# Kernel tuning notes

Hardware: AMD Instinct MI355X
Metric: run time of the kernel (lower is better)

Reference implementation:

```python
import jax, jax.numpy as jnp
import numpy as np

EPS = 1e-7          # K.epsilon()
STRIDE = 1
ROUTINGS = 3


def squash(v, axis=-1):
    # Faithful to original: squash default axis=-1, which for preactivate
    # [B, oc, na, H, W] is the spatial W axis (as the source code computes).
    s2 = jnp.sum(v * v, axis=axis, keepdims=True)
    scale = s2 / (1.0 + s2) / jnp.sqrt(s2 + EPS)
    return scale * v


def setup_inputs() -> dict:
    key = jax.random.key(0)
    k1, k2 = jax.random.split(key, 2)
    B, H, Wd, ic, ia = 32, 32, 32, 8, 16
    k, oc, na = 3, 16, 16
    x = jax.random.normal(k1, (B, H, Wd, ic, ia), jnp.float32)
    # he_normal: std = sqrt(2 / fan_in), fan_in = kd*kh*kw*ci = ia*k*k*1
    std = np.sqrt(2.0 / (ia * k * k)).astype(np.float32)
    W = jax.random.normal(k2, (ia, k, k, 1, oc * na), jnp.float32) * std
    b = jnp.full((oc, na, 1, 1), 0.1, jnp.float32)
    return {"x": x, "W": W, "b": b}


def reference(x, W, b):
    B, H, Wd, ic, ia = x.shape
    oc, na = b.shape[0], b.shape[1]
    # Faithful raw reshape of input_tensor (NOT of input_transposed), as in source.
    xr = x.reshape(B, 1, ic * ia, H, Wd)
    # conv3d channels_first, kernel (kd,kh,kw,ci,co), strides (ia, s, s), valid.
    conv = jax.lax.conv_general_dilated(
        xr, W,
        window_strides=(ia, STRIDE, STRIDE),
        padding='VALID',
        dimension_numbers=('NCDHW', 'DHWIO', 'NCDHW'))
    # conv: [B, oc*na, ic, Hc, Wc]
    _, _, d, Hc, Wc = conv.shape  # d == ic
    votes = jnp.transpose(conv, (0, 2, 1, 3, 4)).reshape(B, ic, oc, na, Hc, Wc)
    biases = jnp.broadcast_to(b, (oc, na, Hc, Wc))
    logits = jnp.zeros((B, ic, oc, Hc, Wc), x.dtype)
    activation = None
    for i in range(ROUTINGS):  # fixed small trip count
        route = jax.nn.softmax(logits, axis=2)           # over output capsules
        # route [B,ic,oc,1,H,W] * votes [B,ic,oc,na,H,W], sum over ic
        preact = jnp.sum(route[:, :, :, None] * votes, axis=1) + biases
        activation = squash(preact, axis=-1)             # [B, oc, na, Hc, Wc]
        if i < ROUTINGS - 1:
            # agreement: sum over atoms axis (axis=3 of votes)
            logits = logits + jnp.sum(votes * activation[:, None], axis=3)
    # final transpose [0,3,4,1,2] -> [B, Hc, Wc, oc, na]
    return jnp.transpose(activation, (0, 3, 4, 1, 2))
```

## Files before the change

### kernel.cpp

```cpp
#include <hip/hip_runtime.h>
#include <hip/hip_bf16.h>

typedef float    f32x4  __attribute__((ext_vector_type(4)));
typedef float    f32x16 __attribute__((ext_vector_type(16)));
typedef _Float16 f16x8  __attribute__((ext_vector_type(8)));
typedef _Float16 f16x4  __attribute__((ext_vector_type(4)));
typedef _Float16 f16x2  __attribute__((ext_vector_type(2)));

#define VP 258
#define XP 132
#define AP 258

__global__ __launch_bounds__(256) void prep_wt_kernel(
    const float* __restrict__ W, _Float16* __restrict__ wt)
{
    const int k = blockIdx.x;
    const int t = threadIdx.x;
    wt[t * 144 + (k % 9) * 16 + (k / 9)] = (_Float16)W[k * 256 + t];
}

__global__ __launch_bounds__(1024, 4) void fused_kernel(
    const float* __restrict__ x, const _Float16* __restrict__ wt,
    const float* __restrict__ bias, float* __restrict__ out)
{
    const int bid = blockIdx.x;
    const int wid = (bid & 7) * 120 + (bid >> 3);
    const int b = wid / 30, h = wid - 30 * b;
    const int t = threadIdx.x;

    __shared__ _Float16 vlds[8 * 30 * VP];
    __shared__ union {
        _Float16 xs[3][36][XP];
        struct {
            _Float16 route16[8 * 16 * 32];
            _Float16 act16[30 * AP];
            float    s2buf[4][256];
        } rt;
    } u;

    {
        const float* xb = x + (size_t)b * 131072;
        f32x4 v0[2], v1[2];
        int p0s[2], rs[2], c4s[2];
        #pragma unroll
        for (int j = 0; j < 2; ++j) {
            int q = t + j * 1024;
            bool ok = q < 1536;
            int qq = ok ? q : 0;
            int g  = qq / 24;
            p0s[j] = g * 2;
            int rem = qq - g * 24;
            rs[j] = rem >> 3; c4s[j] = rem & 7;
            if (ok) {
                v0[j] = *(const f32x4*)(xb + p0s[j] * 1024 + (h + rs[j]) * 32 + c4s[j] * 4);
                v1[j] = *(const f32x4*)(xb + (p0s[j] + 1) * 1024 + (h + rs[j]) * 32 + c4s[j] * 4);
            }
        }
        if (t < 768) {
            int r = t / 256, rem = t - r * 256;
            int c = rem >> 6, pz = (rem & 63) * 2;
            *(f16x2*)&u.xs[r][32 + c][pz] = f16x2{(_Float16)0.f, (_Float16)0.f};
        }
        #pragma unroll
        for (int j = 0; j < 2; ++j) {
            if (t + j * 1024 < 1536) {
                #pragma unroll
                for (int c = 0; c < 4; ++c)
                    *(f16x2*)&u.xs[rs[j]][c4s[j] * 4 + c][p0s[j]] =
                        f16x2{(_Float16)v0[j][c], (_Float16)v1[j][c]};
            }
        }
    }
    __syncthreads();

    const int lane = t & 63, wv = t >> 6;
    const int l31  = lane & 31;
    const int kb   = lane >> 5;
    const int ct   = wv >> 1, dh = wv & 1;
    const int oaC  = ct * 32 + l31;

    {
        f16x8 bf[9];
        const _Float16* wp = wt + (size_t)oaC * 144 + kb * 8;
        #pragma unroll
        for (int s = 0; s < 9; ++s) bf[s] = *(const f16x8*)(wp + s * 16);

        #pragma unroll
        for (int dd = 0; dd < 4; ++dd) {
            f32x16 acc = {};
            #pragma unroll
            for (int s = 0; s < 9; ++s) {
                const int kh = s / 3, kw = s - 3 * (s / 3);
                const _Float16* ap = &u.xs[kh][l31 + kw][dh * 64 + dd * 16 + kb * 8];
                f16x4 lo = *(const f16x4*)(ap);
                f16x4 hi = *(const f16x4*)(ap + 4);
                f16x8 af = __builtin_shufflevector(lo, hi, 0, 1, 2, 3, 4, 5, 6, 7);
                acc = __builtin_amdgcn_mfma_f32_32x32x16_f16(af, bf[s], acc, 0, 0, 0);
            }
            const int d = dh * 4 + dd;
            #pragma unroll
            for (int r = 0; r < 16; ++r) {
                const int wr = (r & 3) + 8 * (r >> 2) + 4 * kb;
                if (wr < 30) vlds[(d * 30 + wr) * VP + oaC] = (_Float16)acc[r];
            }
        }
    }
    __syncthreads();

    const int oa = t & 255, wq = t >> 8;
    const int o  = oa >> 4;
    const int wbase = wq * 8;
    const int nw = (wq == 3) ? 6 : 8;
    const float bias_t = bias[oa];
    const int iA = t / 30, wA = t - iA * 30;

    float lreg[16];
    #pragma unroll
    for (int oo = 0; oo < 16; ++oo) lreg[oo] = 0.f;

    float pre[8];
    float scale = 0.f;

    for (int it = 0; it < 3; ++it) {
        if (it > 0) {
            if (t < 240) {
                float m = lreg[0];
                #pragma unroll
                for (int oo = 1; oo < 16; ++oo) m = fmaxf(m, lreg[oo]);
                float e[16], ssum = 0.f;
                #pragma unroll
                for (int oo = 0; oo < 16; ++oo) { e[oo] = __expf(lreg[oo] - m); ssum += e[oo]; }
                float inv = 1.f / ssum;
                #pragma unroll
                for (int oo = 0; oo < 16; ++oo)
                    u.rt.route16[(iA * 16 + oo) * 32 + wA] = (_Float16)(e[oo] * inv);
            }
            __syncthreads();
        }

        #pragma unroll
        for (int w = 0; w < 8; ++w) pre[w] = bias_t;
        if (it == 0) {
            #pragma unroll
            for (int i = 0; i < 8; ++i) {
                const _Float16* vrow = &vlds[(i * 30 + wbase) * VP + oa];
                #pragma unroll
                for (int w = 0; w < 8; ++w)
                    if (w < nw) pre[w] = fmaf(0.0625f, (float)vrow[w * VP], pre[w]);
            }
        } else {
            #pragma unroll
            for (int i = 0; i < 8; ++i) {
                const _Float16* vrow = &vlds[(i * 30 + wbase) * VP + oa];
                const _Float16* rr   = &u.rt.route16[(i * 16 + o) * 32 + wbase];
                #pragma unroll
                for (int w = 0; w < 8; ++w)
                    if (w < nw) pre[w] = fmaf((float)rr[w], (float)vrow[w * VP], pre[w]);
            }
        }
        float s2p = 0.f;
        #pragma unroll
        for (int w = 0; w < 8; ++w)
            if (w < nw) s2p = fmaf(pre[w], pre[w], s2p);
        u.rt.s2buf[wq][oa] = s2p;
        __syncthreads();
        float s2 = u.rt.s2buf[0][oa] + u.rt.s2buf[1][oa]
                 + u.rt.s2buf[2][oa] + u.rt.s2buf[3][oa];
        scale = s2 / ((1.f + s2) * sqrtf(s2 + 1e-7f));

        if (it < 2) {
            #pragma unroll
            for (int w = 0; w < 8; ++w)
                if (w < nw) u.rt.act16[(wbase + w) * AP + oa] = (_Float16)(scale * pre[w]);
            __syncthreads();
            if (t < 240) {
                const _Float16* vrow = &vlds[(iA * 30 + wA) * VP];
                const _Float16* arow = &u.rt.act16[wA * AP];
                #pragma unroll
                for (int oo = 0; oo < 16; ++oo) {
                    float s = 0.f;
                    #pragma unroll
                    for (int k = 0; k < 8; ++k) {
                        f16x2 v2 = *(const f16x2*)&vrow[oo * 16 + 2 * k];
                        f16x2 a2 = *(const f16x2*)&arow[oo * 16 + 2 * k];
                        s = fmaf((float)v2[0], (float)a2[0], s);
                        s = fmaf((float)v2[1], (float)a2[1], s);
                    }
                    if (it == 0) lreg[oo] = s; else lreg[oo] += s;
                }
            }
        }
    }

    float* ob = out + (size_t)((b * 30 + h) * 30) * 256;
    #pragma unroll
    for (int w = 0; w < 8; ++w)
        if (w < nw) ob[(wbase + w) * 256 + oa] = scale * pre[w];
}

extern "C" void kernel_launch(void* const* d_in, const int* in_sizes, int n_in,
                              void* d_out, int out_size, void* d_ws, size_t ws_size,
                              hipStream_t stream)
{
    const float* x    = (const float*)d_in[0];
    const float* Wt   = (const float*)d_in[1];
    const float* bias = (const float*)d_in[2];
    float* out = (float*)d_out;
    _Float16* wt_h = (_Float16*)d_ws;

    prep_wt_kernel<<<dim3(144), 256, 0, stream>>>(Wt, wt_h);
    fused_kernel<<<dim3(960), 1024, 0, stream>>>(x, wt_h, bias, out);
}
```

Before: 75.87 us.

## Make fused capsule kernel persistent with prefetch of next row's input

```diff
diff --git a/kernel.cpp b/kernel.cpp
--- a/kernel.cpp
+++ b/kernel.cpp
@@ -4,11 +4,10 @@
 typedef float    f32x4  __attribute__((ext_vector_type(4)));
 typedef float    f32x16 __attribute__((ext_vector_type(16)));
 typedef _Float16 f16x8  __attribute__((ext_vector_type(8)));
-typedef _Float16 f16x4  __attribute__((ext_vector_type(4)));
 typedef _Float16 f16x2  __attribute__((ext_vector_type(2)));
 
 #define VP 258
-#define XP 132
+#define XP 136
 #define AP 258
 
 __global__ __launch_bounds__(256) void prep_wt_kernel(
@@ -19,14 +18,13 @@
     wt[t * 144 + (k % 9) * 16 + (k / 9)] = (_Float16)W[k * 256 + t];
 }
 
-__global__ __launch_bounds__(1024, 4) void fused_kernel(
+__global__ __launch_bounds__(1024) void fused_kernel(
     const float* __restrict__ x, const _Float16* __restrict__ wt,
     const float* __restrict__ bias, float* __restrict__ out)
 {
-    const int bid = blockIdx.x;
-    const int wid = (bid & 7) * 120 + (bid >> 3);
-    const int b = wid / 30, h = wid - 30 * b;
-    const int t = threadIdx.x;
+    const int kblk = blockIdx.x;
+    const int t    = threadIdx.x;
+    const int njobs = (kblk < 192) ? 4 : 3;
 
     __shared__ _Float16 vlds[8 * 30 * VP];
     __shared__ union {
@@ -38,52 +36,67 @@
         } rt;
     } u;
 
+    const int lane = t & 63, wv = t >> 6;
+    const int l31 = lane & 31, kb = lane >> 5;
+    const int ct = wv >> 1, dh = wv & 1;
+    const int oaC = ct * 32 + l31;
+
+    const int oa = t & 255, wq = t >> 8;
+    const int o = oa >> 4;
+    const int wbase = wq * 8;
+    const int nw = (wq == 3) ? 6 : 8;
+    const float bias_t = bias[oa];
+    const int iA = t / 30, wA = t - iA * 30;
+
+    const bool ok1 = (t < 512);
+    const int g0 = t / 24,          p00 = g0 * 2;
+    const int rem0 = t - g0 * 24,   r0 = rem0 >> 3, c40 = rem0 & 7;
+    const int q1 = t + 1024;
+    const int g1 = q1 / 24,         p01 = g1 * 2;
+    const int rem1 = q1 - g1 * 24,  r1 = rem1 >> 3, c41 = rem1 & 7;
+
+    f16x8 bf[9];
     {
+        const _Float16* wp = wt + (size_t)oaC * 144 + kb * 8;
+        #pragma unroll
+        for (int s = 0; s < 9; ++s) bf[s] = *(const f16x8*)(wp + s * 16);
+    }
+
+    f32x4 v00, v01, v10, v11;
+    {
+        const int j = kblk;
+        const int wid = (j & 7) * 120 + (j >> 3);
+        const int b = wid / 30, h = wid - 30 * b;
         const float* xb = x + (size_t)b * 131072;
-        f32x4 v0[2], v1[2];
-        int p0s[2], rs[2], c4s[2];
-        #pragma unroll
-        for (int j = 0; j < 2; ++j) {
-            int q = t + j * 1024;
-            bool ok = q < 1536;
-            int qq = ok ? q : 0;
-            int g  = qq / 24;
-            p0s[j] = g * 2;
-            int rem = qq - g * 24;
-            rs[j] = rem >> 3; c4s[j] = rem & 7;
-            if (ok) {
-                v0[j] = *(const f32x4*)(xb + p0s[j] * 1024 + (h + rs[j]) * 32 + c4s[j] * 4);
-                v1[j] = *(const f32x4*)(xb + (p0s[j] + 1) * 1024 + (h + rs[j]) * 32 + c4s[j] * 4);
-            }
-        }
+        v00 = *(const f32x4*)(xb + p00 * 1024 + (h + r0) * 32 + c40 * 4);
+        v01 = *(const f32x4*)(xb + (p00 + 1) * 1024 + (h + r0) * 32 + c40 * 4);
+        if (ok1) {
+            v10 = *(const f32x4*)(xb + p01 * 1024 + (h + r1) * 32 + c41 * 4);
+            v11 = *(const f32x4*)(xb + (p01 + 1) * 1024 + (h + r1) * 32 + c41 * 4);
+        }
+    }
+
+    for (int jj = 0; jj < njobs; ++jj) {
+        const int j = kblk + jj * 256;
+        const int wid = (j & 7) * 120 + (j >> 3);
+        const int b = wid / 30, h = wid - 30 * b;
+
+        if (jj > 0) __syncthreads();
+
         if (t < 768) {
             int r = t / 256, rem = t - r * 256;
             int c = rem >> 6, pz = (rem & 63) * 2;
             *(f16x2*)&u.xs[r][32 + c][pz] = f16x2{(_Float16)0.f, (_Float16)0.f};
         }
         #pragma unroll
-        for (int j = 0; j < 2; ++j) {
-            if (t + j * 1024 < 1536) {
-                #pragma unroll
-                for (int c = 0; c < 4; ++c)
-                    *(f16x2*)&u.xs[rs[j]][c4s[j] * 4 + c][p0s[j]] =
-                        f16x2{(_Float16)v0[j][c], (_Float16)v1[j][c]};
-            }
-        }
-    }
-    __syncthreads();
-
-    const int lane = t & 63, wv = t >> 6;
-    const int l31  = lane & 31;
-    const int kb   = lane >> 5;
-    const int ct   = wv >> 1, dh = wv & 1;
-    const int oaC  = ct * 32 + l31;
-
-    {
-        f16x8 bf[9];
-        const _Float16* wp = wt + (size_t)oaC * 144 + kb * 8;
-        #pragma unroll
-        for (int s = 0; s < 9; ++s) bf[s] = *(const f16x8*)(wp + s * 16);
+        for (int c = 0; c < 4; ++c)
+            *(f16x2*)&u.xs[r0][c40 * 4 + c][p00] = f16x2{(_Float16)v00[c], (_Float16)v01[c]};
+        if (ok1) {
+            #pragma unroll
+            for (int c = 0; c < 4; ++c)
+                *(f16x2*)&u.xs[r1][c41 * 4 + c][p01] = f16x2{(_Float16)v10[c], (_Float16)v11[c]};
+        }
+        __syncthreads();
 
         #pragma unroll
         for (int dd = 0; dd < 4; ++dd) {
@@ -91,10 +104,7 @@
             #pragma unroll
             for (int s = 0; s < 9; ++s) {
                 const int kh = s / 3, kw = s - 3 * (s / 3);
-                const _Float16* ap = &u.xs[kh][l31 + kw][dh * 64 + dd * 16 + kb * 8];
-                f16x4 lo = *(const f16x4*)(ap);
-                f16x4 hi = *(const f16x4*)(ap + 4);
-                f16x8 af = __builtin_shufflevector(lo, hi, 0, 1, 2, 3, 4, 5, 6, 7);
+                f16x8 af = *(const f16x8*)&u.xs[kh][l31 + kw][dh * 64 + dd * 16 + kb * 8];
                 acc = __builtin_amdgcn_mfma_f32_32x32x16_f16(af, bf[s], acc, 0, 0, 0);
             }
             const int d = dh * 4 + dd;
@@ -104,98 +114,105 @@
                 if (wr < 30) vlds[(d * 30 + wr) * VP + oaC] = (_Float16)acc[r];
             }
         }
-    }
-    __syncthreads();
-
-    const int oa = t & 255, wq = t >> 8;
-    const int o  = oa >> 4;
-    const int wbase = wq * 8;
-    const int nw = (wq == 3) ? 6 : 8;
-    const float bias_t = bias[oa];
-    const int iA = t / 30, wA = t - iA * 30;
-
-    float lreg[16];
-    #pragma unroll
-    for (int oo = 0; oo < 16; ++oo) lreg[oo] = 0.f;
-
-    float pre[8];
-    float scale = 0.f;
-
-    for (int it = 0; it < 3; ++it) {
-        if (it > 0) {
-            if (t < 240) {
-                float m = lreg[0];
+        __syncthreads();
+
+        if (jj + 1 < njobs) {
+            const int jn = kblk + (jj + 1) * 256;
+            const int widn = (jn & 7) * 120 + (jn >> 3);
+            const int bn = widn / 30, hn = widn - 30 * bn;
+            const float* xb = x + (size_t)bn * 131072;
+            v00 = *(const f32x4*)(xb + p00 * 1024 + (hn + r0) * 32 + c40 * 4);
+            v01 = *(const f32x4*)(xb + (p00 + 1) * 1024 + (hn + r0) * 32 + c40 * 4);
+            if (ok1) {
+                v10 = *(const f32x4*)(xb + p01 * 1024 + (hn + r1) * 32 + c41 * 4);
+                v11 = *(const f32x4*)(xb + (p01 + 1) * 1024 + (hn + r1) * 32 + c41 * 4);
+            }
+        }
+
+        float lreg[16];
+        float pre[8];
+        float scale = 0.f;
+
+        for (int it = 0; it < 3; ++it) {
+            if (it > 0) {
+                if (t < 240) {
+                    float m = lreg[0];
+                    #pragma unroll
+                    for (int oo = 1; oo < 16; ++oo) m = fmaxf(m, lreg[oo]);
+                    float e[16], ssum = 0.f;
+                    #pragma unroll
+                    for (int oo = 0; oo < 16; ++oo) { e[oo] = __expf(lreg[oo] - m); ssum += e[oo]; }
+                    float inv = 1.f / ssum;
+                    #pragma unroll
+                    for (int oo = 0; oo < 16; ++oo)
+                        u.rt.route16[(iA * 16 + oo) * 32 + wA] = (_Float16)(e[oo] * inv);
+                }
+                __syncthreads();
+            }
+
+            #pragma unroll
+            for (int w = 0; w < 8; ++w) pre[w] = bias_t;
+            if (it == 0) {
                 #pragma unroll
-                for (int oo = 1; oo < 16; ++oo) m = fmaxf(m, lreg[oo]);
-                float e[16], ssum = 0.f;
+                for (int i = 0; i < 8; ++i) {
+                    const _Float16* vrow = &vlds[(i * 30 + wbase) * VP + oa];
+                    #pragma unroll
+                    for (int w = 0; w < 8; ++w)
+                        if (w < nw) pre[w] = fmaf(0.0625f, (float)vrow[w * VP], pre[w]);
+                }
+            } else {
                 #pragma unroll
-                for (int oo = 0; oo < 16; ++oo) { e[oo] = __expf(lreg[oo] - m); ssum += e[oo]; }
-                float inv = 1.f / ssum;
-                #pragma unroll
-                for (int oo = 0; oo < 16; ++oo)
-                    u.rt.route16[(iA * 16 + oo) * 32 + wA] = (_Float16)(e[oo] * inv);
-            }
+                for (int i = 0; i < 8; ++i) {
+                    const _Float16* vrow = &vlds[(i * 30 + wbase) * VP + oa];
+                    const _Float16* rr   = &u.rt.route16[(i * 16 + o) * 32 + wbase];
+                    #pragma unroll
+                    for (int w = 0; w < 8; ++w)
+                        if (w < nw) pre[w] = fmaf((float)rr[w], (float)vrow[w * VP], pre[w]);
+                }
+            }
+            float s2p = 0.f;
+            #pragma unroll
+            for (int w = 0; w < 8; ++w)
+                if (w < nw) s2p = fmaf(pre[w], pre[w], s2p);
+            u.rt.s2buf[wq][oa] = s2p;
             __syncthreads();
-        }
-
-        #pragma unroll
-        for (int w = 0; w < 8; ++w) pre[w] = bias_t;
-        if (it == 0) {
-            #pragma unroll
-            for (int i = 0; i < 8; ++i) {
-                const _Float16* vrow = &vlds[(i * 30 + wbase) * VP + oa];
+            float s2 = u.rt.s2buf[0][oa] + u.rt.s2buf[1][oa]
+                     + u.rt.s2buf[2][oa] + u.rt.s2buf[3][oa];
+            scale = s2 / ((1.f + s2) * sqrtf(s2 + 1e-7f));
+
+            if (it < 2) {
                 #pragma unroll
                 for (int w = 0; w < 8; ++w)
-                    if (w < nw) pre[w] = fmaf(0.0625f, (float)vrow[w * VP], pre[w]);
-            }
-        } else {
-            #pragma unroll
-            for (int i = 0; i < 8; ++i) {
-                const _Float16* vrow = &vlds[(i * 30 + wbase) * VP + oa];
-                const _Float16* rr   = &u.rt.route16[(i * 16 + o) * 32 + wbase];
-                #pragma unroll
-                for (int w = 0; w < 8; ++w)
-                    if (w < nw) pre[w] = fmaf((float)rr[w], (float)vrow[w * VP], pre[w]);
-            }
-        }
-        float s2p = 0.f;
+                    if (w < nw) u.rt.act16[(wbase + w) * AP + oa] = (_Float16)(scale * pre[w]);
+                __syncthreads();
+                if (t < 240) {
+                    const _Float16* vrow = &vlds[(iA * 30 + wA) * VP];
+                    const _Float16* arow = &u.rt.act16[wA * AP];
+                    #pragma unroll
+                    for (int oo = 0; oo < 16; ++oo) {
+                        float s = 0.f;
+                        #pragma unroll
+                        for (int kk = 0; kk < 8; ++kk) {
+                            f16x2 v2 = *(const f16x2*)&vrow[oo * 16 + 2 * kk];
+                            f16x2 a2 = *(const f16x2*)&arow[oo * 16 + 2 * kk];
+#if __has_builtin(__builtin_amdgcn_fdot2)
+                            s = __builtin_amdgcn_fdot2(v2, a2, s, false);
+#else
+                            s = fmaf((float)v2[0], (float)a2[0], s);
+                            s = fmaf((float)v2[1], (float)a2[1], s);
+#endif
+                        }
+                        if (it == 0) lreg[oo] = s; else lreg[oo] += s;
+                    }
+                }
+            }
+        }
+
+        float* ob = out + (size_t)((b * 30 + h) * 30) * 256;
         #pragma unroll
         for (int w = 0; w < 8; ++w)
-            if (w < nw) s2p = fmaf(pre[w], pre[w], s2p);
-        u.rt.s2buf[wq][oa] = s2p;
-        __syncthreads();
-        float s2 = u.rt.s2buf[0][oa] + u.rt.s2buf[1][oa]
-                 + u.rt.s2buf[2][oa] + u.rt.s2buf[3][oa];
-        scale = s2 / ((1.f + s2) * sqrtf(s2 + 1e-7f));
-
-        if (it < 2) {
-            #pragma unroll
-            for (int w = 0; w < 8; ++w)
-                if (w < nw) u.rt.act16[(wbase + w) * AP + oa] = (_Float16)(scale * pre[w]);
-            __syncthreads();
-            if (t < 240) {
-                const _Float16* vrow = &vlds[(iA * 30 + wA) * VP];
-                const _Float16* arow = &u.rt.act16[wA * AP];
-                #pragma unroll
-                for (int oo = 0; oo < 16; ++oo) {
-                    float s = 0.f;
-                    #pragma unroll
-                    for (int k = 0; k < 8; ++k) {
-                        f16x2 v2 = *(const f16x2*)&vrow[oo * 16 + 2 * k];
-                        f16x2 a2 = *(const f16x2*)&arow[oo * 16 + 2 * k];
-                        s = fmaf((float)v2[0], (float)a2[0], s);
-                        s = fmaf((float)v2[1], (float)a2[1], s);
-                    }
-                    if (it == 0) lreg[oo] = s; else lreg[oo] += s;
-                }
-            }
-        }
+            if (w < nw) ob[(wbase + w) * 256 + oa] = scale * pre[w];
     }
-
-    float* ob = out + (size_t)((b * 30 + h) * 30) * 256;
-    #pragma unroll
-    for (int w = 0; w < 8; ++w)
-        if (w < nw) ob[(wbase + w) * 256 + oa] = scale * pre[w];
 }
 
 extern "C" void kernel_launch(void* const* d_in, const int* in_sizes, int n_in,
@@ -209,5 +226,5 @@
     _Float16* wt_h = (_Float16*)d_ws;
 
     prep_wt_kernel<<<dim3(144), 256, 0, stream>>>(Wt, wt_h);
-    fused_kernel<<<dim3(960), 1024, 0, stream>>>(x, wt_h, bias, out);
+    fused_kernel<<<dim3(256), 1024, 0, stream>>>(x, wt_h, bias, out);
 }
```

Result: slower. 179.2 us (+136.3%).

## Remap routing phase to two atoms per thread with vectorized LDS and fdot2

Applied to the files above, without the earlier changes.

```diff
diff --git a/kernel.cpp b/kernel.cpp
--- a/kernel.cpp
+++ b/kernel.cpp
@@ -1,15 +1,17 @@
 #include <hip/hip_runtime.h>
 #include <hip/hip_bf16.h>
 
+typedef float    f32x2  __attribute__((ext_vector_type(2)));
 typedef float    f32x4  __attribute__((ext_vector_type(4)));
 typedef float    f32x16 __attribute__((ext_vector_type(16)));
 typedef _Float16 f16x8  __attribute__((ext_vector_type(8)));
 typedef _Float16 f16x4  __attribute__((ext_vector_type(4)));
 typedef _Float16 f16x2  __attribute__((ext_vector_type(2)));
 
-#define VP 258
+#define VP 264
 #define XP 132
-#define AP 258
+#define AP 264
+#define RP 36
 
 __global__ __launch_bounds__(256) void prep_wt_kernel(
     const float* __restrict__ W, _Float16* __restrict__ wt)
@@ -28,13 +30,13 @@
     const int b = wid / 30, h = wid - 30 * b;
     const int t = threadIdx.x;
 
-    __shared__ _Float16 vlds[8 * 30 * VP];
-    __shared__ union {
+    __shared__ alignas(16) _Float16 vlds[8 * 30 * VP];
+    __shared__ alignas(16) union {
         _Float16 xs[3][36][XP];
         struct {
-            _Float16 route16[8 * 16 * 32];
+            _Float16 route16[8 * 16 * RP];
             _Float16 act16[30 * AP];
-            float    s2buf[4][256];
+            f32x2    s2buf[8][128];
         } rt;
     } u;
 
@@ -107,19 +109,20 @@
     }
     __syncthreads();
 
-    const int oa = t & 255, wq = t >> 8;
-    const int o  = oa >> 4;
-    const int wbase = wq * 8;
-    const int nw = (wq == 3) ? 6 : 8;
-    const float bias_t = bias[oa];
+    const int oa2 = t & 127;
+    const int wq8 = t >> 7;
+    const int wbase = wq8 * 4;
+    const int nw = (wq8 == 7) ? 2 : 4;
+    const int o = oa2 >> 3;
+    const float biasA = bias[2 * oa2], biasB = bias[2 * oa2 + 1];
     const int iA = t / 30, wA = t - iA * 30;
+    bool wok[4];
+    #pragma unroll
+    for (int w = 0; w < 4; ++w) wok[w] = (wbase + w) < 30;
 
     float lreg[16];
-    #pragma unroll
-    for (int oo = 0; oo < 16; ++oo) lreg[oo] = 0.f;
-
-    float pre[8];
-    float scale = 0.f;
+    float preA[4], preB[4];
+    float scaleA = 0.f, scaleB = 0.f;
 
     for (int it = 0; it < 3; ++it) {
         if (it > 0) {
@@ -133,58 +136,85 @@
                 float inv = 1.f / ssum;
                 #pragma unroll
                 for (int oo = 0; oo < 16; ++oo)
-                    u.rt.route16[(iA * 16 + oo) * 32 + wA] = (_Float16)(e[oo] * inv);
+                    u.rt.route16[(iA * 16 + oo) * RP + wA] = (_Float16)(e[oo] * inv);
             }
             __syncthreads();
         }
 
         #pragma unroll
-        for (int w = 0; w < 8; ++w) pre[w] = bias_t;
-        if (it == 0) {
-            #pragma unroll
-            for (int i = 0; i < 8; ++i) {
-                const _Float16* vrow = &vlds[(i * 30 + wbase) * VP + oa];
-                #pragma unroll
-                for (int w = 0; w < 8; ++w)
-                    if (w < nw) pre[w] = fmaf(0.0625f, (float)vrow[w * VP], pre[w]);
-            }
-        } else {
-            #pragma unroll
-            for (int i = 0; i < 8; ++i) {
-                const _Float16* vrow = &vlds[(i * 30 + wbase) * VP + oa];
-                const _Float16* rr   = &u.rt.route16[(i * 16 + o) * 32 + wbase];
-                #pragma unroll
-                for (int w = 0; w < 8; ++w)
-                    if (w < nw) pre[w] = fmaf((float)rr[w], (float)vrow[w * VP], pre[w]);
-            }
-        }
-        float s2p = 0.f;
-        #pragma unroll
-        for (int w = 0; w < 8; ++w)
-            if (w < nw) s2p = fmaf(pre[w], pre[w], s2p);
-        u.rt.s2buf[wq][oa] = s2p;
+        for (int w = 0; w < 4; ++w) { preA[w] = biasA; preB[w] = biasB; }
+        #pragma unroll
+        for (int i = 0; i < 8; ++i) {
+            f16x2 vv[4];
+            #pragma unroll
+            for (int w = 0; w < 4; ++w)
+                vv[w] = wok[w] ? *(const f16x2*)&vlds[(i * 30 + wbase + w) * VP + 2 * oa2]
+                               : f16x2{(_Float16)0.f, (_Float16)0.f};
+            if (it == 0) {
+                #pragma unroll
+                for (int w = 0; w < 4; ++w) {
+                    preA[w] = fmaf(0.0625f, (float)vv[w][0], preA[w]);
+                    preB[w] = fmaf(0.0625f, (float)vv[w][1], preB[w]);
+                }
+            } else {
+                f16x4 r4 = *(const f16x4*)&u.rt.route16[(i * 16 + o) * RP + wbase];
+                #pragma unroll
+                for (int w = 0; w < 4; ++w) {
+                    float rw = (float)r4[w];
+                    preA[w] = fmaf(rw, (float)vv[w][0], preA[w]);
+                    preB[w] = fmaf(rw, (float)vv[w][1], preB[w]);
+                }
+            }
+        }
+        float s2A = 0.f, s2B = 0.f;
+        #pragma unroll
+        for (int w = 0; w < 4; ++w) {
+            if (wok[w]) {
+                s2A = fmaf(preA[w], preA[w], s2A);
+                s2B = fmaf(preB[w], preB[w], s2B);
+            }
+        }
+        u.rt.s2buf[wq8][oa2] = f32x2{s2A, s2B};
         __syncthreads();
-        float s2 = u.rt.s2buf[0][oa] + u.rt.s2buf[1][oa]
-                 + u.rt.s2buf[2][oa] + u.rt.s2buf[3][oa];
-        scale = s2 / ((1.f + s2) * sqrtf(s2 + 1e-7f));
+        float sA = 0.f, sB = 0.f;
+        #pragma unroll
+        for (int k = 0; k < 8; ++k) {
+            f32x2 p = u.rt.s2buf[k][oa2];
+            sA += p[0]; sB += p[1];
+        }
+        scaleA = sA / ((1.f + sA) * sqrtf(sA + 1e-7f));
+        scaleB = sB / ((1.f + sB) * sqrtf(sB + 1e-7f));
 
         if (it < 2) {
             #pragma unroll
-            for (int w = 0; w < 8; ++w)
-                if (w < nw) u.rt.act16[(wbase + w) * AP + oa] = (_Float16)(scale * pre[w]);
+            for (int w = 0; w < 4; ++w)
+                if (wok[w])
+                    *(f16x2*)&u.rt.act16[(wbase + w) * AP + 2 * oa2] =
+                        f16x2{(_Float16)(scaleA * preA[w]), (_Float16)(scaleB * preB[w])};
             __syncthreads();
             if (t < 240) {
                 const _Float16* vrow = &vlds[(iA * 30 + wA) * VP];
                 const _Float16* arow = &u.rt.act16[wA * AP];
                 #pragma unroll
                 for (int oo = 0; oo < 16; ++oo) {
+                    f16x8 v0 = *(const f16x8*)&vrow[oo * 16];
+                    f16x8 v1 = *(const f16x8*)&vrow[oo * 16 + 8];
+                    f16x8 a0 = *(const f16x8*)&arow[oo * 16];
+                    f16x8 a1 = *(const f16x8*)&arow[oo * 16 + 8];
                     float s = 0.f;
                     #pragma unroll
-                    for (int k = 0; k < 8; ++k) {
-                        f16x2 v2 = *(const f16x2*)&vrow[oo * 16 + 2 * k];
-                        f16x2 a2 = *(const f16x2*)&arow[oo * 16 + 2 * k];
-                        s = fmaf((float)v2[0], (float)a2[0], s);
-                        s = fmaf((float)v2[1], (float)a2[1], s);
+                    for (int kk = 0; kk < 4; ++kk) {
+#if __has_builtin(__builtin_amdgcn_fdot2)
+                        s = __builtin_amdgcn_fdot2(f16x2{v0[2 * kk], v0[2 * kk + 1]},
+                                                   f16x2{a0[2 * kk], a0[2 * kk + 1]}, s, false);
+                        s = __builtin_amdgcn_fdot2(f16x2{v1[2 * kk], v1[2 * kk + 1]},
+                                                   f16x2{a1[2 * kk], a1[2 * kk + 1]}, s, false);
+#else
+                        s = fmaf((float)v0[2 * kk], (float)a0[2 * kk], s);
+                        s = fmaf((float)v0[2 * kk + 1], (float)a0[2 * kk + 1], s);
+                        s = fmaf((float)v1[2 * kk], (float)a1[2 * kk], s);
+                        s = fmaf((float)v1[2 * kk + 1], (float)a1[2 * kk + 1], s);
+#endif
                     }
                     if (it == 0) lreg[oo] = s; else lreg[oo] += s;
                 }
@@ -194,8 +224,10 @@
 
     float* ob = out + (size_t)((b * 30 + h) * 30) * 256;
     #pragma unroll
-    for (int w = 0; w < 8; ++w)
-        if (w < nw) ob[(wbase + w) * 256 + oa] = scale * pre[w];
+    for (int w = 0; w < 4; ++w)
+        if (wok[w])
+            *(f32x2*)&ob[(wbase + w) * 256 + 2 * oa2] =
+                f32x2{scaleA * preA[w], scaleB * preB[w]};
 }
 
 extern "C" void kernel_launch(void* const* d_in, const int* in_sizes, int n_in,
```

Result: faster. 67.61 us (-10.9%).
